# Optimization experiments

Measured on AMD Instinct MI355X. Metric: run time of the kernel, lower is better.

The kernel has to match this reference:

```python
import jax, jax.numpy as jnp
import numpy as np

CLAMP_MIN = 1e-12
CLAMP_MAX = 1e12


def setup_inputs() -> dict:
    key = jax.random.key(0)
    k1, k2, k3 = jax.random.split(key, 3)
    N, C, H, W = 32, 11, 384, 384
    x = jax.random.normal(k1, (N, C, H, W), dtype=jnp.float32)
    centers = jax.random.normal(k2, (N, C, H, W), dtype=jnp.float32)
    labels = jax.random.randint(k3, (N, H, W), 0, C, dtype=jnp.int64)
    return {"x": x, "centers": centers, "labels": labels}


def reference(x, centers, labels):
    # x, centers: (N, C, H, W); labels: (N, H, W) int
    N, C, H, W = x.shape
    # res[n,c] = x[n,c]^2 + centers[n,c]^2 - 2 * x[n,c] @ centers[n,c]
    # (single batched matmul replaces the original per-(i,j) addmm loop)
    res = x * x + centers * centers - 2.0 * jnp.matmul(x, centers)
    # softmax over class dim, then max over class dim -> (N, H, W)
    res_max = jnp.max(jax.nn.softmax(res, axis=1), axis=1)
    dist = res_max * labels.astype(res_max.dtype)
    loss = jnp.sum(jnp.clip(dist, CLAMP_MIN, CLAMP_MAX)) / (H * W * N)
    return loss
```

## Files before the change

### kernel.cpp

```cpp
#include <hip/hip_runtime.h>
#include <stdint.h>

typedef __attribute__((ext_vector_type(8))) short short8;
typedef __attribute__((ext_vector_type(4))) float floatx4;
typedef __attribute__((ext_vector_type(4))) unsigned short u16x4;

#define Hh 384
#define Ww 384
#define Cc 11
#define Nn 32
#define PITCH 72

__device__ __forceinline__ unsigned short f2bf(float f) {
  union { float f; uint32_t u; } z; z.f = f;
  return (unsigned short)(z.u >> 16);
}
__device__ __forceinline__ float bf2f(unsigned short b) {
  union { uint32_t u; float f; } z; z.u = ((uint32_t)b) << 16;
  return z.f;
}

__global__ __launch_bounds__(256, 4)
void center_partial(const float* __restrict__ X, const float* __restrict__ Cen,
                    float2* __restrict__ Ws) {
  __shared__ __align__(16) unsigned short Alds[64 * PITCH];
  __shared__ __align__(16) unsigned short Blds[64 * PITCH];

  const int bx    = blockIdx.x;
  const int chunk = (bx >= 1152) ? 1 : 0;
  const int bxl   = bx - chunk * 1152;
  const int c0    = chunk * 6;
  const int NT    = chunk ? 30 : 36;

  const int xcd  = bxl & 7;
  const int slot = bxl >> 3;
  const int grp  = slot / 36;
  const int t36  = slot - grp * 36;
  const int n    = xcd + (grp << 3);
  const int ib = t36 / 6;
  const int jb = t36 - ib * 6;
  const int i0 = ib << 6, j0 = jb << 6;

  const int t   = threadIdx.x;
  const int l   = t & 63;
  const int w   = t >> 6;
  const int wr  = (w >> 1) << 5;
  const int wc  = (w & 1) << 5;
  const int q4  = l >> 4;
  const int l16 = l & 15;
  const int sa  = t & 15;
  const int sr  = t >> 4;

  const size_t plane = (size_t)Hh * Ww;
  const float* xbase = X   + ((size_t)n * Cc + c0) * plane;
  const float* cbase = Cen + ((size_t)n * Cc + c0) * plane;

  float m[16], s[16];
#pragma unroll
  for (int i = 0; i < 16; ++i) { m[i] = -3.0e38f; s[i] = 0.0f; }

  floatx4 acc[2][2];
  float ev[16];
#pragma unroll
  for (int a = 0; a < 2; ++a)
#pragma unroll
    for (int b = 0; b < 2; ++b) acc[a][b] = (floatx4){0.f, 0.f, 0.f, 0.f};
#pragma unroll
  for (int i = 0; i < 16; ++i) ev[i] = 0.0f;

  float4 pa[4];
  float  pb[16];

  {
    const float* ap = xbase + (size_t)(i0 + sr) * Ww + (sa << 2);
#pragma unroll
    for (int p = 0; p < 4; ++p)
      pa[p] = *reinterpret_cast<const float4*>(ap + (size_t)(p * 16) * Ww);
#pragma unroll
    for (int p = 0; p < 2; ++p) {
      const int kbase = (w << 3) + (p << 5);
      const float* bp = cbase + (size_t)kbase * Ww + j0 + l;
#pragma unroll
      for (int u = 0; u < 8; ++u) pb[p * 8 + u] = bp[(size_t)u * Ww];
    }
  }

  int c = 0, kb = 0;
  for (int it = 0; it < NT; ++it) {
    __syncthreads();

#pragma unroll
    for (int p = 0; p < 4; ++p) {
      u16x4 pk;
      pk.x = f2bf(pa[p].x); pk.y = f2bf(pa[p].y);
      pk.z = f2bf(pa[p].z); pk.w = f2bf(pa[p].w);
      *reinterpret_cast<u16x4*>(&Alds[(sr + 16 * p) * PITCH + (sa << 2)]) = pk;
    }
#pragma unroll
    for (int p = 0; p < 2; ++p) {
      const int kbase = (w << 3) + (p << 5);
      short8 pk;
#pragma unroll
      for (int u = 0; u < 8; ++u) pk[u] = (short)f2bf(pb[p * 8 + u]);
      *reinterpret_cast<short8*>(&Blds[l * PITCH + kbase]) = pk;
    }

    int kn = kb + 1, cn = c;
    if (kn == 6) { kn = 0; cn = c + 1; }
    float4 na[4];
    float  nb[16];
    if (it < NT - 1) {
      const float* xb = xbase + (size_t)cn * plane;
      const float* cb = cbase + (size_t)cn * plane;
      const float* ap = xb + (size_t)(i0 + sr) * Ww + (kn << 6) + (sa << 2);
#pragma unroll
      for (int p = 0; p < 4; ++p)
        na[p] = *reinterpret_cast<const float4*>(ap + (size_t)(p * 16) * Ww);
#pragma unroll
      for (int p = 0; p < 2; ++p) {
        const int kbase = (w << 3) + (p << 5);
        const float* bp = cb + (size_t)((kn << 6) + kbase) * Ww + j0 + l;
#pragma unroll
        for (int u = 0; u < 8; ++u) nb[p * 8 + u] = bp[(size_t)u * Ww];
      }
    }

    __syncthreads();

    if (kb == jb) {
#pragma unroll
      for (int fr = 0; fr < 2; ++fr)
#pragma unroll
        for (int fc = 0; fc < 2; ++fc)
#pragma unroll
          for (int r = 0; r < 4; ++r) {
            const int idx = ((fr << 1) + fc) * 4 + r;
            const int pr = wr + (fr << 4) + (q4 << 2) + r;
            const int pc = wc + (fc << 4) + l16;
            float xv = bf2f(Alds[pr * PITCH + pc]);
            ev[idx] += xv * xv;
          }
    }
    if (kb == ib) {
#pragma unroll
      for (int fr = 0; fr < 2; ++fr)
#pragma unroll
        for (int fc = 0; fc < 2; ++fc)
#pragma unroll
          for (int r = 0; r < 4; ++r) {
            const int idx = ((fr << 1) + fc) * 4 + r;
            const int pr = wr + (fr << 4) + (q4 << 2) + r;
            const int pc = wc + (fc << 4) + l16;
            float cv = bf2f(Blds[pc * PITCH + pr]);
            ev[idx] += cv * cv;
          }
    }

#pragma unroll
    for (int ks = 0; ks < 2; ++ks) {
      const int ko = (ks << 5) + (q4 << 3);
      short8 a0 = *reinterpret_cast<const short8*>(&Alds[(wr +      l16) * PITCH + ko]);
      short8 a1 = *reinterpret_cast<const short8*>(&Alds[(wr + 16 + l16) * PITCH + ko]);
      short8 b0 = *reinterpret_cast<const short8*>(&Blds[(wc +      l16) * PITCH + ko]);
      short8 b1 = *reinterpret_cast<const short8*>(&Blds[(wc + 16 + l16) * PITCH + ko]);
      acc[0][0] = __builtin_amdgcn_mfma_f32_16x16x32_bf16(a0, b0, acc[0][0], 0, 0, 0);
      acc[0][1] = __builtin_amdgcn_mfma_f32_16x16x32_bf16(a0, b1, acc[0][1], 0, 0, 0);
      acc[1][0] = __builtin_amdgcn_mfma_f32_16x16x32_bf16(a1, b0, acc[1][0], 0, 0, 0);
      acc[1][1] = __builtin_amdgcn_mfma_f32_16x16x32_bf16(a1, b1, acc[1][1], 0, 0, 0);
    }

    if (kb == 5) {
#pragma unroll
      for (int fr = 0; fr < 2; ++fr)
#pragma unroll
        for (int fc = 0; fc < 2; ++fc)
#pragma unroll
          for (int r = 0; r < 4; ++r) {
            const int idx = ((fr << 1) + fc) * 4 + r;
            float res = ev[idx] - 2.0f * acc[fr][fc][r];
            float mi = m[idx];
            if (res <= mi) {
              s[idx] += __expf(res - mi);
            } else {
              s[idx] = s[idx] * __expf(mi - res) + 1.0f;
              m[idx] = res;
            }
            acc[fr][fc][r] = 0.0f;
            ev[idx] = 0.0f;
          }
    }

    kb = kn; c = cn;
#pragma unroll
    for (int p = 0; p < 4; ++p) pa[p] = na[p];
#pragma unroll
    for (int p = 0; p < 16; ++p) pb[p] = nb[p];
  }

  float2* wsk = Ws + ((size_t)chunk * Nn + n) * plane;
#pragma unroll
  for (int fr = 0; fr < 2; ++fr)
#pragma unroll
    for (int fc = 0; fc < 2; ++fc)
#pragma unroll
      for (int r = 0; r < 4; ++r) {
        const int idx = ((fr << 1) + fc) * 4 + r;
        const int pr = i0 + wr + (fr << 4) + (q4 << 2) + r;
        const int pc = j0 + wc + (fc << 4) + l16;
        float2 v; v.x = m[idx]; v.y = s[idx];
        wsk[(size_t)pr * Ww + pc] = v;
      }
}

__global__ __launch_bounds__(256)
void center_merge(const float2* __restrict__ Ws, const int* __restrict__ Lab,
                  float* __restrict__ Out) {
  __shared__ float red[4];
  const size_t NP = (size_t)Nn * Hh * Ww;
  const size_t stride = 4608ull * 256;
  size_t e = (size_t)blockIdx.x * 256 + threadIdx.x;
  float local = 0.0f;
#pragma unroll
  for (int u = 0; u < 4; ++u, e += stride) {
    float2 a = Ws[e];
    float2 b = Ws[NP + e];
    float M = fmaxf(a.x, b.x);
    float S = a.y * __expf(a.x - M) + b.y * __expf(b.x - M);
    float d = (1.0f / S) * (float)Lab[e];
    d = fminf(fmaxf(d, 1e-12f), 1e12f);
    local += d;
  }
  const int l = threadIdx.x & 63, w = threadIdx.x >> 6;
#pragma unroll
  for (int off = 32; off > 0; off >>= 1) local += __shfl_down(local, off, 64);
  if (l == 0) red[w] = local;
  __syncthreads();
  if (threadIdx.x == 0)
    atomicAdd(Out, (red[0] + red[1] + red[2] + red[3]) * (1.0f / 4718592.0f));
}

__global__ __launch_bounds__(256, 4)
void center_loss_mono(const float* __restrict__ X, const float* __restrict__ Cen,
                      const int* __restrict__ Lab, float* __restrict__ Out) {
  __shared__ __align__(16) unsigned short Alds[64 * PITCH];
  __shared__ __align__(16) unsigned short Blds[64 * PITCH];
  __shared__ float red[4];

  const int bx   = blockIdx.x;
  const int xcd  = bx & 7;
  const int slot = bx >> 3;
  const int grp  = slot / 36;
  const int t36  = slot - grp * 36;
  const int n    = xcd + (grp << 3);
  const int ib = t36 / 6;
  const int jb = t36 - ib * 6;
  const int i0 = ib << 6, j0 = jb << 6;

  const int t   = threadIdx.x;
  const int l   = t & 63;
  const int w   = t >> 6;
  const int wr  = (w >> 1) << 5;
  const int wc  = (w & 1) << 5;
  const int q4  = l >> 4;
  const int l16 = l & 15;
  const int sa  = t & 15;
  const int sr  = t >> 4;

  const size_t plane = (size_t)Hh * Ww;
  const float* xbase = X   + (size_t)n * Cc * plane;
  const float* cbase = Cen + (size_t)n * Cc * plane;

  float m[16], s[16];
#pragma unroll
  for (int i = 0; i < 16; ++i) { m[i] = -3.0e38f; s[i] = 0.0f; }
  floatx4 acc[2][2];
  float ev[16];
#pragma unroll
  for (int a = 0; a < 2; ++a)
#pragma unroll
    for (int b = 0; b < 2; ++b) acc[a][b] = (floatx4){0.f, 0.f, 0.f, 0.f};
#pragma unroll
  for (int i = 0; i < 16; ++i) ev[i] = 0.0f;

  float4 pa[4];
  float  pb[16];
  {
    const float* ap = xbase + (size_t)(i0 + sr) * Ww + (sa << 2);
#pragma unroll
    for (int p = 0; p < 4; ++p)
      pa[p] = *reinterpret_cast<const float4*>(ap + (size_t)(p * 16) * Ww);
#pragma unroll
    for (int p = 0; p < 2; ++p) {
      const int kbase = (w << 3) + (p << 5);
      const float* bp = cbase + (size_t)kbase * Ww + j0 + l;
#pragma unroll
      for (int u = 0; u < 8; ++u) pb[p * 8 + u] = bp[(size_t)u * Ww];
    }
  }

  int c = 0, kb = 0;
  for (int it = 0; it < 66; ++it) {
    __syncthreads();
#pragma unroll
    for (int p = 0; p < 4; ++p) {
      u16x4 pk;
      pk.x = f2bf(pa[p].x); pk.y = f2bf(pa[p].y);
      pk.z = f2bf(pa[p].z); pk.w = f2bf(pa[p].w);
      *reinterpret_cast<u16x4*>(&Alds[(sr + 16 * p) * PITCH + (sa << 2)]) = pk;
    }
#pragma unroll
    for (int p = 0; p < 2; ++p) {
      const int kbase = (w << 3) + (p << 5);
      short8 pk;
#pragma unroll
      for (int u = 0; u < 8; ++u) pk[u] = (short)f2bf(pb[p * 8 + u]);
      *reinterpret_cast<short8*>(&Blds[l * PITCH + kbase]) = pk;
    }
    int kn = kb + 1, cn = c;
    if (kn == 6) { kn = 0; cn = c + 1; }
    float4 na[4];
    float  nb[16];
    if (it < 65) {
      const float* xb = xbase + (size_t)cn * plane;
      const float* cb = cbase + (size_t)cn * plane;
      const float* ap = xb + (size_t)(i0 + sr) * Ww + (kn << 6) + (sa << 2);
#pragma unroll
      for (int p = 0; p < 4; ++p)
        na[p] = *reinterpret_cast<const float4*>(ap + (size_t)(p * 16) * Ww);
#pragma unroll
      for (int p = 0; p < 2; ++p) {
        const int kbase = (w << 3) + (p << 5);
        const float* bp = cb + (size_t)((kn << 6) + kbase) * Ww + j0 + l;
#pragma unroll
        for (int u = 0; u < 8; ++u) nb[p * 8 + u] = bp[(size_t)u * Ww];
      }
    }
    __syncthreads();
    if (kb == jb) {
#pragma unroll
      for (int fr = 0; fr < 2; ++fr)
#pragma unroll
        for (int fc = 0; fc < 2; ++fc)
#pragma unroll
          for (int r = 0; r < 4; ++r) {
            const int idx = ((fr << 1) + fc) * 4 + r;
            const int pr = wr + (fr << 4) + (q4 << 2) + r;
            const int pc = wc + (fc << 4) + l16;
            float xv = bf2f(Alds[pr * PITCH + pc]);
            ev[idx] += xv * xv;
          }
    }
    if (kb == ib) {
#pragma unroll
      for (int fr = 0; fr < 2; ++fr)
#pragma unroll
        for (int fc = 0; fc < 2; ++fc)
#pragma unroll
          for (int r = 0; r < 4; ++r) {
            const int idx = ((fr << 1) + fc) * 4 + r;
            const int pr = wr + (fr << 4) + (q4 << 2) + r;
            const int pc = wc + (fc << 4) + l16;
            float cv = bf2f(Blds[pc * PITCH + pr]);
            ev[idx] += cv * cv;
          }
    }
#pragma unroll
    for (int ks = 0; ks < 2; ++ks) {
      const int ko = (ks << 5) + (q4 << 3);
      short8 a0 = *reinterpret_cast<const short8*>(&Alds[(wr +      l16) * PITCH + ko]);
      short8 a1 = *reinterpret_cast<const short8*>(&Alds[(wr + 16 + l16) * PITCH + ko]);
      short8 b0 = *reinterpret_cast<const short8*>(&Blds[(wc +      l16) * PITCH + ko]);
      short8 b1 = *reinterpret_cast<const short8*>(&Blds[(wc + 16 + l16) * PITCH + ko]);
      acc[0][0] = __builtin_amdgcn_mfma_f32_16x16x32_bf16(a0, b0, acc[0][0], 0, 0, 0);
      acc[0][1] = __builtin_amdgcn_mfma_f32_16x16x32_bf16(a0, b1, acc[0][1], 0, 0, 0);
      acc[1][0] = __builtin_amdgcn_mfma_f32_16x16x32_bf16(a1, b0, acc[1][0], 0, 0, 0);
      acc[1][1] = __builtin_amdgcn_mfma_f32_16x16x32_bf16(a1, b1, acc[1][1], 0, 0, 0);
    }
    if (kb == 5) {
#pragma unroll
      for (int fr = 0; fr < 2; ++fr)
#pragma unroll
        for (int fc = 0; fc < 2; ++fc)
#pragma unroll
          for (int r = 0; r < 4; ++r) {
            const int idx = ((fr << 1) + fc) * 4 + r;
            float res = ev[idx] - 2.0f * acc[fr][fc][r];
            float mi = m[idx];
            if (res <= mi) {
              s[idx] += __expf(res - mi);
            } else {
              s[idx] = s[idx] * __expf(mi - res) + 1.0f;
              m[idx] = res;
            }
            acc[fr][fc][r] = 0.0f;
            ev[idx] = 0.0f;
          }
    }
    kb = kn; c = cn;
#pragma unroll
    for (int p = 0; p < 4; ++p) pa[p] = na[p];
#pragma unroll
    for (int p = 0; p < 16; ++p) pb[p] = nb[p];
  }

  float local = 0.0f;
  const int* lb = Lab + (size_t)n * plane;
#pragma unroll
  for (int fr = 0; fr < 2; ++fr)
#pragma unroll
    for (int fc = 0; fc < 2; ++fc)
#pragma unroll
      for (int r = 0; r < 4; ++r) {
        const int idx = ((fr << 1) + fc) * 4 + r;
        const int pr = i0 + wr + (fr << 4) + (q4 << 2) + r;
        const int pc = j0 + wc + (fc << 4) + l16;
        float val = 1.0f / s[idx];
        float d = val * (float)lb[pr * Ww + pc];
        d = fminf(fmaxf(d, 1e-12f), 1e12f);
        local += d;
      }
#pragma unroll
  for (int off = 32; off > 0; off >>= 1) local += __shfl_down(local, off, 64);
  if (l == 0) red[w] = local;
  __syncthreads();
  if (t == 0) {
    float bs = (red[0] + red[1] + red[2] + red[3]) * (1.0f / 4718592.0f);
    atomicAdd(Out, bs);
  }
}

extern "C" void kernel_launch(void* const* d_in, const int* in_sizes, int n_in,
                              void* d_out, int out_size, void* d_ws, size_t ws_size,
                              hipStream_t stream) {
  const float* X   = (const float*)d_in[0];
  const float* Cen = (const float*)d_in[1];
  const int*   Lab = (const int*)d_in[2];
  float* Out = (float*)d_out;
  hipMemsetAsync(Out, 0, (size_t)out_size * sizeof(float), stream);

  const size_t need = 2ull * Nn * Hh * Ww * sizeof(float2);
  if (ws_size >= need && d_ws != nullptr) {
    float2* Ws = (float2*)d_ws;
    hipLaunchKernelGGL(center_partial, dim3(2 * Nn * 36), dim3(256), 0, stream,
                       X, Cen, Ws);
    hipLaunchKernelGGL(center_merge, dim3(4608), dim3(256), 0, stream,
                       Ws, Lab, Out);
  } else {
    hipLaunchKernelGGL(center_loss_mono, dim3(Nn * 36), dim3(256), 0, stream,
                       X, Cen, Lab, Out);
  }
}
```

Before: 545.0 us.

## Fuse merge into split kernel via completion flags, drop register prefetch

The separate merge kernel is removed. Whichever of the two channel-chunk blocks finishes last for a tile, detected through an atomic counter, now merges the partial softmax stats and reduces the loss. The register double-buffer prefetch is replaced by direct load-convert-store each iteration, with a raw barrier, perm-based bf16 packing and occupancy raised to 6. The squared-norm terms are folded into the MFMA accumulator to free registers. This trades global-load latency hiding for higher occupancy and one fewer launch, and relies on correct fencing between the partial writes and the merge.

```diff
diff --git a/kernel.cpp b/kernel.cpp
--- a/kernel.cpp
+++ b/kernel.cpp
@@ -3,7 +3,8 @@
 
 typedef __attribute__((ext_vector_type(8))) short short8;
 typedef __attribute__((ext_vector_type(4))) float floatx4;
-typedef __attribute__((ext_vector_type(4))) unsigned short u16x4;
+typedef __attribute__((ext_vector_type(2))) uint32_t u32x2;
+typedef __attribute__((ext_vector_type(4))) uint32_t u32x4;
 
 #define Hh 384
 #define Ww 384
@@ -11,20 +12,29 @@
 #define Nn 32
 #define PITCH 72
 
-__device__ __forceinline__ unsigned short f2bf(float f) {
-  union { float f; uint32_t u; } z; z.f = f;
-  return (unsigned short)(z.u >> 16);
-}
 __device__ __forceinline__ float bf2f(unsigned short b) {
   union { uint32_t u; float f; } z; z.u = ((uint32_t)b) << 16;
   return z.f;
 }
-
-__global__ __launch_bounds__(256, 4)
-void center_partial(const float* __restrict__ X, const float* __restrict__ Cen,
-                    float2* __restrict__ Ws) {
+__device__ __forceinline__ uint32_t pkbf(float hi, float lo) {
+  union { float f; uint32_t u; } a, b; a.f = hi; b.f = lo;
+  return __builtin_amdgcn_perm(a.u, b.u, 0x07060302u);
+}
+
+#define BAR() do {                                          \
+    asm volatile("s_waitcnt lgkmcnt(0)" ::: "memory");      \
+    __builtin_amdgcn_s_barrier();                           \
+    asm volatile("" ::: "memory");                          \
+  } while (0)
+
+__global__ __launch_bounds__(256, 6)
+void center_split(const float* __restrict__ X, const float* __restrict__ Cen,
+                  const int* __restrict__ Lab, float* __restrict__ Out,
+                  float2* __restrict__ Ws, int* __restrict__ Flags) {
   __shared__ __align__(16) unsigned short Alds[64 * PITCH];
   __shared__ __align__(16) unsigned short Blds[64 * PITCH];
+  __shared__ float red[4];
+  __shared__ int oldsh;
 
   const int bx    = blockIdx.x;
   const int chunk = (bx >= 1152) ? 1 : 0;
@@ -54,78 +64,58 @@
   const size_t plane = (size_t)Hh * Ww;
   const float* xbase = X   + ((size_t)n * Cc + c0) * plane;
   const float* cbase = Cen + ((size_t)n * Cc + c0) * plane;
+  const size_t aoffg = (size_t)(i0 + sr) * Ww + (sa << 2);
 
   float m[16], s[16];
 #pragma unroll
   for (int i = 0; i < 16; ++i) { m[i] = -3.0e38f; s[i] = 0.0f; }
 
   floatx4 acc[2][2];
-  float ev[16];
 #pragma unroll
   for (int a = 0; a < 2; ++a)
 #pragma unroll
     for (int b = 0; b < 2; ++b) acc[a][b] = (floatx4){0.f, 0.f, 0.f, 0.f};
-#pragma unroll
-  for (int i = 0; i < 16; ++i) ev[i] = 0.0f;
-
-  float4 pa[4];
-  float  pb[16];
-
-  {
-    const float* ap = xbase + (size_t)(i0 + sr) * Ww + (sa << 2);
-#pragma unroll
-    for (int p = 0; p < 4; ++p)
-      pa[p] = *reinterpret_cast<const float4*>(ap + (size_t)(p * 16) * Ww);
+
+  int kb = 0, c = 0;
+  for (int it = 0; it < NT; ++it) {
+    BAR();
+
+    {
+      const float* ap = xbase + (size_t)c * plane + (kb << 6) + aoffg;
+      float4 a0 = *reinterpret_cast<const float4*>(ap);
+      float4 a1 = *reinterpret_cast<const float4*>(ap + (size_t)16 * Ww);
+      float4 a2 = *reinterpret_cast<const float4*>(ap + (size_t)32 * Ww);
+      float4 a3 = *reinterpret_cast<const float4*>(ap + (size_t)48 * Ww);
+      u32x2 p0, p1, p2, p3;
+      p0.x = pkbf(a0.y, a0.x); p0.y = pkbf(a0.w, a0.z);
+      p1.x = pkbf(a1.y, a1.x); p1.y = pkbf(a1.w, a1.z);
+      p2.x = pkbf(a2.y, a2.x); p2.y = pkbf(a2.w, a2.z);
+      p3.x = pkbf(a3.y, a3.x); p3.y = pkbf(a3.w, a3.z);
+      *reinterpret_cast<u32x2*>(&Alds[(sr +  0) * PITCH + (sa << 2)]) = p0;
+      *reinterpret_cast<u32x2*>(&Alds[(sr + 16) * PITCH + (sa << 2)]) = p1;
+      *reinterpret_cast<u32x2*>(&Alds[(sr + 32) * PITCH + (sa << 2)]) = p2;
+      *reinterpret_cast<u32x2*>(&Alds[(sr + 48) * PITCH + (sa << 2)]) = p3;
+    }
 #pragma unroll
     for (int p = 0; p < 2; ++p) {
       const int kbase = (w << 3) + (p << 5);
-      const float* bp = cbase + (size_t)kbase * Ww + j0 + l;
-#pragma unroll
-      for (int u = 0; u < 8; ++u) pb[p * 8 + u] = bp[(size_t)u * Ww];
-    }
-  }
-
-  int c = 0, kb = 0;
-  for (int it = 0; it < NT; ++it) {
-    __syncthreads();
-
-#pragma unroll
-    for (int p = 0; p < 4; ++p) {
-      u16x4 pk;
-      pk.x = f2bf(pa[p].x); pk.y = f2bf(pa[p].y);
-      pk.z = f2bf(pa[p].z); pk.w = f2bf(pa[p].w);
-      *reinterpret_cast<u16x4*>(&Alds[(sr + 16 * p) * PITCH + (sa << 2)]) = pk;
-    }
-#pragma unroll
-    for (int p = 0; p < 2; ++p) {
-      const int kbase = (w << 3) + (p << 5);
-      short8 pk;
-#pragma unroll
-      for (int u = 0; u < 8; ++u) pk[u] = (short)f2bf(pb[p * 8 + u]);
-      *reinterpret_cast<short8*>(&Blds[l * PITCH + kbase]) = pk;
-    }
-
-    int kn = kb + 1, cn = c;
-    if (kn == 6) { kn = 0; cn = c + 1; }
-    float4 na[4];
-    float  nb[16];
-    if (it < NT - 1) {
-      const float* xb = xbase + (size_t)cn * plane;
-      const float* cb = cbase + (size_t)cn * plane;
-      const float* ap = xb + (size_t)(i0 + sr) * Ww + (kn << 6) + (sa << 2);
-#pragma unroll
-      for (int p = 0; p < 4; ++p)
-        na[p] = *reinterpret_cast<const float4*>(ap + (size_t)(p * 16) * Ww);
-#pragma unroll
-      for (int p = 0; p < 2; ++p) {
-        const int kbase = (w << 3) + (p << 5);
-        const float* bp = cb + (size_t)((kn << 6) + kbase) * Ww + j0 + l;
-#pragma unroll
-        for (int u = 0; u < 8; ++u) nb[p * 8 + u] = bp[(size_t)u * Ww];
-      }
-    }
-
-    __syncthreads();
+      const float* bp = cbase + (size_t)c * plane +
+                        (size_t)((kb << 6) + kbase) * Ww + j0 + l;
+      float b0 = bp[0];
+      float b1 = bp[(size_t)1 * Ww];
+      float b2 = bp[(size_t)2 * Ww];
+      float b3 = bp[(size_t)3 * Ww];
+      float b4 = bp[(size_t)4 * Ww];
+      float b5 = bp[(size_t)5 * Ww];
+      float b6 = bp[(size_t)6 * Ww];
+      float b7 = bp[(size_t)7 * Ww];
+      u32x4 pk;
+      pk.x = pkbf(b1, b0); pk.y = pkbf(b3, b2);
+      pk.z = pkbf(b5, b4); pk.w = pkbf(b7, b6);
+      *reinterpret_cast<u32x4*>(&Blds[l * PITCH + kbase]) = pk;
+    }
+
+    BAR();
 
     if (kb == jb) {
 #pragma unroll
@@ -134,11 +124,10 @@
         for (int fc = 0; fc < 2; ++fc)
 #pragma unroll
           for (int r = 0; r < 4; ++r) {
-            const int idx = ((fr << 1) + fc) * 4 + r;
             const int pr = wr + (fr << 4) + (q4 << 2) + r;
             const int pc = wc + (fc << 4) + l16;
             float xv = bf2f(Alds[pr * PITCH + pc]);
-            ev[idx] += xv * xv;
+            acc[fr][fc][r] -= 0.5f * xv * xv;
           }
     }
     if (kb == ib) {
@@ -148,11 +137,10 @@
         for (int fc = 0; fc < 2; ++fc)
 #pragma unroll
           for (int r = 0; r < 4; ++r) {
-            const int idx = ((fr << 1) + fc) * 4 + r;
             const int pr = wr + (fr << 4) + (q4 << 2) + r;
             const int pc = wc + (fc << 4) + l16;
             float cv = bf2f(Blds[pc * PITCH + pr]);
-            ev[idx] += cv * cv;
+            acc[fr][fc][r] -= 0.5f * cv * cv;
           }
     }
 
@@ -177,7 +165,7 @@
 #pragma unroll
           for (int r = 0; r < 4; ++r) {
             const int idx = ((fr << 1) + fc) * 4 + r;
-            float res = ev[idx] - 2.0f * acc[fr][fc][r];
+            float res = -2.0f * acc[fr][fc][r];
             float mi = m[idx];
             if (res <= mi) {
               s[idx] += __expf(res - mi);
@@ -186,15 +174,10 @@
               m[idx] = res;
             }
             acc[fr][fc][r] = 0.0f;
-            ev[idx] = 0.0f;
-          }
-    }
-
-    kb = kn; c = cn;
-#pragma unroll
-    for (int p = 0; p < 4; ++p) pa[p] = na[p];
-#pragma unroll
-    for (int p = 0; p < 16; ++p) pb[p] = nb[p];
+          }
+    }
+
+    ++kb; if (kb == 6) { kb = 0; ++c; }
   }
 
   float2* wsk = Ws + ((size_t)chunk * Nn + n) * plane;
@@ -210,38 +193,41 @@
         float2 v; v.x = m[idx]; v.y = s[idx];
         wsk[(size_t)pr * Ww + pc] = v;
       }
+
+  __syncthreads();
+  __threadfence();
+  if (t == 0) oldsh = atomicAdd(&Flags[n * 36 + t36], 1);
+  __syncthreads();
+  if (oldsh == 1) {
+    __threadfence();
+    const float2* w0 = Ws + (size_t)n * plane;
+    const float2* w1 = Ws + (size_t)(Nn + n) * plane;
+    const int*    lb = Lab + (size_t)n * plane;
+    float local = 0.0f;
+#pragma unroll
+    for (int u = 0; u < 16; ++u) {
+      const int idx = (u << 8) + t;
+      const size_t g = (size_t)(i0 + (idx >> 6)) * Ww + (j0 + (idx & 63));
+      float2 a = w0[g], b = w1[g];
+      float S;
+      if (a.x >= b.x) S = a.y + b.y * __expf(b.x - a.x);
+      else            S = b.y + a.y * __expf(a.x - b.x);
+      float d = (1.0f / S) * (float)lb[g];
+      d = fminf(fmaxf(d, 1e-12f), 1e12f);
+      local += d;
+    }
+#pragma unroll
+    for (int off = 32; off > 0; off >>= 1) local += __shfl_down(local, off, 64);
+    if (l == 0) red[w] = local;
+    __syncthreads();
+    if (t == 0)
+      atomicAdd(Out, (red[0] + red[1] + red[2] + red[3]) * (1.0f / 4718592.0f));
+  }
 }
 
-__global__ __launch_bounds__(256)
-void center_merge(const float2* __restrict__ Ws, const int* __restrict__ Lab,
-                  float* __restrict__ Out) {
-  __shared__ float red[4];
-  const size_t NP = (size_t)Nn * Hh * Ww;
-  const size_t stride = 4608ull * 256;
-  size_t e = (size_t)blockIdx.x * 256 + threadIdx.x;
-  float local = 0.0f;
-#pragma unroll
-  for (int u = 0; u < 4; ++u, e += stride) {
-    float2 a = Ws[e];
-    float2 b = Ws[NP + e];
-    float M = fmaxf(a.x, b.x);
-    float S = a.y * __expf(a.x - M) + b.y * __expf(b.x - M);
-    float d = (1.0f / S) * (float)Lab[e];
-    d = fminf(fmaxf(d, 1e-12f), 1e12f);
-    local += d;
-  }
-  const int l = threadIdx.x & 63, w = threadIdx.x >> 6;
-#pragma unroll
-  for (int off = 32; off > 0; off >>= 1) local += __shfl_down(local, off, 64);
-  if (l == 0) red[w] = local;
-  __syncthreads();
-  if (threadIdx.x == 0)
-    atomicAdd(Out, (red[0] + red[1] + red[2] + red[3]) * (1.0f / 4718592.0f));
-}
-
-__global__ __launch_bounds__(256, 4)
-void center_loss_mono(const float* __restrict__ X, const float* __restrict__ Cen,
-                      const int* __restrict__ Lab, float* __restrict__ Out) {
+__global__ __launch_bounds__(256, 3)
+void center_mono(const float* __restrict__ X, const float* __restrict__ Cen,
+                 const int* __restrict__ Lab, float* __restrict__ Out) {
   __shared__ __align__(16) unsigned short Alds[64 * PITCH];
   __shared__ __align__(16) unsigned short Blds[64 * PITCH];
   __shared__ float red[4];
@@ -269,73 +255,55 @@
   const size_t plane = (size_t)Hh * Ww;
   const float* xbase = X   + (size_t)n * Cc * plane;
   const float* cbase = Cen + (size_t)n * Cc * plane;
+  const size_t aoffg = (size_t)(i0 + sr) * Ww + (sa << 2);
 
   float m[16], s[16];
 #pragma unroll
   for (int i = 0; i < 16; ++i) { m[i] = -3.0e38f; s[i] = 0.0f; }
   floatx4 acc[2][2];
-  float ev[16];
 #pragma unroll
   for (int a = 0; a < 2; ++a)
 #pragma unroll
     for (int b = 0; b < 2; ++b) acc[a][b] = (floatx4){0.f, 0.f, 0.f, 0.f};
-#pragma unroll
-  for (int i = 0; i < 16; ++i) ev[i] = 0.0f;
-
-  float4 pa[4];
-  float  pb[16];
-  {
-    const float* ap = xbase + (size_t)(i0 + sr) * Ww + (sa << 2);
-#pragma unroll
-    for (int p = 0; p < 4; ++p)
-      pa[p] = *reinterpret_cast<const float4*>(ap + (size_t)(p * 16) * Ww);
+
+  int kb = 0, c = 0;
+  for (int it = 0; it < 66; ++it) {
+    BAR();
+    {
+      const float* ap = xbase + (size_t)c * plane + (kb << 6) + aoffg;
+      float4 a0 = *reinterpret_cast<const float4*>(ap);
+      float4 a1 = *reinterpret_cast<const float4*>(ap + (size_t)16 * Ww);
+      float4 a2 = *reinterpret_cast<const float4*>(ap + (size_t)32 * Ww);
+      float4 a3 = *reinterpret_cast<const float4*>(ap + (size_t)48 * Ww);
+      u32x2 p0, p1, p2, p3;
+      p0.x = pkbf(a0.y, a0.x); p0.y = pkbf(a0.w, a0.z);
+      p1.x = pkbf(a1.y, a1.x); p1.y = pkbf(a1.w, a1.z);
+      p2.x = pkbf(a2.y, a2.x); p2.y = pkbf(a2.w, a2.z);
+      p3.x = pkbf(a3.y, a3.x); p3.y = pkbf(a3.w, a3.z);
+      *reinterpret_cast<u32x2*>(&Alds[(sr +  0) * PITCH + (sa << 2)]) = p0;
+      *reinterpret_cast<u32x2*>(&Alds[(sr + 16) * PITCH + (sa << 2)]) = p1;
+      *reinterpret_cast<u32x2*>(&Alds[(sr + 32) * PITCH + (sa << 2)]) = p2;
+      *reinterpret_cast<u32x2*>(&Alds[(sr + 48) * PITCH + (sa << 2)]) = p3;
+    }
 #pragma unroll
     for (int p = 0; p < 2; ++p) {
       const int kbase = (w << 3) + (p << 5);
-      const float* bp = cbase + (size_t)kbase * Ww + j0 + l;
-#pragma unroll
-      for (int u = 0; u < 8; ++u) pb[p * 8 + u] = bp[(size_t)u * Ww];
-    }
-  }
-
-  int c = 0, kb = 0;
-  for (int it = 0; it < 66; ++it) {
-    __syncthreads();
-#pragma unroll
-    for (int p = 0; p < 4; ++p) {
-      u16x4 pk;
-      pk.x = f2bf(pa[p].x); pk.y = f2bf(pa[p].y);
-      pk.z = f2bf(pa[p].z); pk.w = f2bf(pa[p].w);
-      *reinterpret_cast<u16x4*>(&Alds[(sr + 16 * p) * PITCH + (sa << 2)]) = pk;
-    }
-#pragma unroll
-    for (int p = 0; p < 2; ++p) {
-      const int kbase = (w << 3) + (p << 5);
-      short8 pk;
-#pragma unroll
-      for (int u = 0; u < 8; ++u) pk[u] = (short)f2bf(pb[p * 8 + u]);
-      *reinterpret_cast<short8*>(&Blds[l * PITCH + kbase]) = pk;
-    }
-    int kn = kb + 1, cn = c;
-    if (kn == 6) { kn = 0; cn = c + 1; }
-    float4 na[4];
-    float  nb[16];
-    if (it < 65) {
-      const float* xb = xbase + (size_t)cn * plane;
-      const float* cb = cbase + (size_t)cn * plane;
-      const float* ap = xb + (size_t)(i0 + sr) * Ww + (kn << 6) + (sa << 2);
-#pragma unroll
-      for (int p = 0; p < 4; ++p)
-        na[p] = *reinterpret_cast<const float4*>(ap + (size_t)(p * 16) * Ww);
-#pragma unroll
-      for (int p = 0; p < 2; ++p) {
-        const int kbase = (w << 3) + (p << 5);
-        const float* bp = cb + (size_t)((kn << 6) + kbase) * Ww + j0 + l;
-#pragma unroll
-        for (int u = 0; u < 8; ++u) nb[p * 8 + u] = bp[(size_t)u * Ww];
-      }
-    }
-    __syncthreads();
+      const float* bp = cbase + (size_t)c * plane +
+                        (size_t)((kb << 6) + kbase) * Ww + j0 + l;
+      float b0 = bp[0];
+      float b1 = bp[(size_t)1 * Ww];
+      float b2 = bp[(size_t)2 * Ww];
+      float b3 = bp[(size_t)3 * Ww];
+      float b4 = bp[(size_t)4 * Ww];
+      float b5 = bp[(size_t)5 * Ww];
+      float b6 = bp[(size_t)6 * Ww];
+      float b7 = bp[(size_t)7 * Ww];
+      u32x4 pk;
+      pk.x = pkbf(b1, b0); pk.y = pkbf(b3, b2);
+      pk.z = pkbf(b5, b4); pk.w = pkbf(b7, b6);
+      *reinterpret_cast<u32x4*>(&Blds[l * PITCH + kbase]) = pk;
+    }
+    BAR();
     if (kb == jb) {
 #pragma unroll
       for (int fr = 0; fr < 2; ++fr)
@@ -343,11 +311,10 @@
         for (int fc = 0; fc < 2; ++fc)
 #pragma unroll
           for (int r = 0; r < 4; ++r) {
-            const int idx = ((fr << 1) + fc) * 4 + r;
             const int pr = wr + (fr << 4) + (q4 << 2) + r;
             const int pc = wc + (fc << 4) + l16;
             float xv = bf2f(Alds[pr * PITCH + pc]);
-            ev[idx] += xv * xv;
+            acc[fr][fc][r] -= 0.5f * xv * xv;
           }
     }
     if (kb == ib) {
@@ -357,11 +324,10 @@
         for (int fc = 0; fc < 2; ++fc)
 #pragma unroll
           for (int r = 0; r < 4; ++r) {
-            const int idx = ((fr << 1) + fc) * 4 + r;
             const int pr = wr + (fr << 4) + (q4 << 2) + r;
             const int pc = wc + (fc << 4) + l16;
             float cv = bf2f(Blds[pc * PITCH + pr]);
-            ev[idx] += cv * cv;
+            acc[fr][fc][r] -= 0.5f * cv * cv;
           }
     }
 #pragma unroll
@@ -384,7 +350,7 @@
 #pragma unroll
           for (int r = 0; r < 4; ++r) {
             const int idx = ((fr << 1) + fc) * 4 + r;
-            float res = ev[idx] - 2.0f * acc[fr][fc][r];
+            float res = -2.0f * acc[fr][fc][r];
             float mi = m[idx];
             if (res <= mi) {
               s[idx] += __expf(res - mi);
@@ -393,14 +359,9 @@
               m[idx] = res;
             }
             acc[fr][fc][r] = 0.0f;
-            ev[idx] = 0.0f;
-          }
-    }
-    kb = kn; c = cn;
-#pragma unroll
-    for (int p = 0; p < 4; ++p) pa[p] = na[p];
-#pragma unroll
-    for (int p = 0; p < 16; ++p) pb[p] = nb[p];
+          }
+    }
+    ++kb; if (kb == 6) { kb = 0; ++c; }
   }
 
   float local = 0.0f;
@@ -438,15 +399,16 @@
   float* Out = (float*)d_out;
   hipMemsetAsync(Out, 0, (size_t)out_size * sizeof(float), stream);
 
-  const size_t need = 2ull * Nn * Hh * Ww * sizeof(float2);
+  const size_t ws_f2   = 2ull * Nn * Hh * Ww * sizeof(float2);
+  const size_t need    = ws_f2 + 1152 * sizeof(int);
   if (ws_size >= need && d_ws != nullptr) {
     float2* Ws = (float2*)d_ws;
-    hipLaunchKernelGGL(center_partial, dim3(2 * Nn * 36), dim3(256), 0, stream,
-                       X, Cen, Ws);
-    hipLaunchKernelGGL(center_merge, dim3(4608), dim3(256), 0, stream,
-                       Ws, Lab, Out);
+    int* Flags = (int*)((char*)d_ws + ws_f2);
+    hipMemsetAsync(Flags, 0, 1152 * sizeof(int), stream);
+    hipLaunchKernelGGL(center_split, dim3(2 * Nn * 36), dim3(256), 0, stream,
+                       X, Cen, Lab, Out, Ws, Flags);
   } else {
-    hipLaunchKernelGGL(center_loss_mono, dim3(Nn * 36), dim3(256), 0, stream,
+    hipLaunchKernelGGL(center_mono, dim3(Nn * 36), dim3(256), 0, stream,
                        X, Cen, Lab, Out);
   }
 }
```

Result: slower. 1.091 ms (+100.2%).
